# Kernel tuning notes

Measured on AMD Instinct MI355X. Metric: run time of the kernel, lower is better.

The kernel has to match this reference:

```python
import jax, jax.numpy as jnp
import numpy as np

N = 100000   # cells per k-dimension
C = 64       # input channels per dim
H = 128      # hidden dim
NNZ = 800000 # nonzeros per sparse matrix (avg degree 8)


def spmm(r, c, v, x):
    # y = A @ x for COO A with rows r, cols c, vals v; x: [N, H]
    return jax.ops.segment_sum(v[:, None] * x[c], r, num_segments=x.shape[0])


def spmm_t(r, c, v, y):
    # z = A.T @ y
    return jax.ops.segment_sum(v[:, None] * y[r], c, num_segments=y.shape[0])


def encoder(xs, params, adjs, B1, B2):
    # HierarchicalMessagePassing over k-dims 0..2; boundary_down[k]=B_k, boundary_up[k]=B_{k+1}
    bdown = (None, B1, B2)
    bup = (B1, B2, None)
    outs = []
    for d in range(3):
        W, b, a = params[d]
        xt = xs[d] @ W + b                                   # [N, H]
        ar, ac, av = adjs[d]
        comb = spmm(ar, ac, av, xt)                          # same-dim messages
        if bdown[d] is not None:
            r, c, v = bdown[d]
            comb = comb + 0.5 * spmm_t(r, c, v, spmm(r, c, v, xt))
        if bup[d] is not None:
            r, c, v = bup[d]
            comb = comb + 0.5 * spmm_t(r, c, v, spmm(r, c, v, xt))
        gate = jax.nn.sigmoid(comb @ a)                      # [N] sigmoid attention
        outs.append(gate[:, None] * comb)
    return jnp.mean(jnp.stack(outs, 0), 0)                   # mean over k-dims


def setup_inputs() -> dict:
    key = jax.random.key(0)
    ks = iter(jax.random.split(key, 64))
    d = {}
    for i in range(3):
        d[f"x{i}"] = jax.random.normal(next(ks), (N, C), jnp.float32)
    for nm in ("a0", "a1", "a2", "b1", "b2"):
        d[nm + "r"] = jax.random.randint(next(ks), (NNZ,), 0, N, jnp.int32)
        d[nm + "c"] = jax.random.randint(next(ks), (NNZ,), 0, N, jnp.int32)
        d[nm + "v"] = jax.random.uniform(next(ks), (NNZ,), jnp.float32)
    sw = 1.0 / np.sqrt(C)
    sh = 1.0 / np.sqrt(H)
    for tag in ("o", "t"):
        for i in range(3):
            d[f"W{tag}{i}"] = jax.random.normal(next(ks), (C, H), jnp.float32) * sw
            d[f"b{tag}{i}"] = jnp.zeros((H,), jnp.float32)
            d[f"a{tag}{i}"] = jax.random.normal(next(ks), (H,), jnp.float32) * 0.1
    d["pW1"] = jax.random.normal(next(ks), (H, H), jnp.float32) * sh
    d["pb1"] = jnp.zeros((H,), jnp.float32)
    d["alpha"] = jnp.full((1,), 0.25, jnp.float32)  # PReLU default
    d["pW2"] = jax.random.normal(next(ks), (H, H), jnp.float32) * sh
    d["pb2"] = jnp.zeros((H,), jnp.float32)
    return d


def reference(x0, x1, x2, a0r, a0c, a0v, a1r, a1c, a1v, a2r, a2c, a2v,
              b1r, b1c, b1v, b2r, b2c, b2v,
              Wo0, bo0, ao0, Wo1, bo1, ao1, Wo2, bo2, ao2,
              Wt0, bt0, at0, Wt1, bt1, at1, Wt2, bt2, at2,
              pW1, pb1, alpha, pW2, pb2):
    xs = (x0, x1, x2)
    adjs = ((a0r, a0c, a0v), (a1r, a1c, a1v), (a2r, a2c, a2v))
    B1 = (b1r, b1c, b1v)
    B2 = (b2r, b2c, b2v)
    h_online = encoder(xs, ((Wo0, bo0, ao0), (Wo1, bo1, ao1), (Wo2, bo2, ao2)), adjs, B1, B2)
    h1 = h_online @ pW1 + pb1
    h1 = jnp.where(h1 >= 0, h1, alpha * h1)  # PReLU
    h_pred = h1 @ pW2 + pb2
    h_target = jax.lax.stop_gradient(
        encoder(xs, ((Wt0, bt0, at0), (Wt1, bt1, at1), (Wt2, bt2, at2)), adjs, B1, B2))
    return h_online, h_pred, h_target
```

## Files before the change

kernel.cpp:

```cpp
#include <hip/hip_runtime.h>
#include <cstddef>

#define NCELL 100000
#define NNZE  800000
#define HID   128
#define CIN   64
#define T7    (7 * NCELL)
#define KPB   512
#define NBKT  196
#define TOTB  (7 * NBKT)

struct P7i { const int* p[7]; };
struct P7f { const float* p[7]; };

__device__ __forceinline__ unsigned short f2bf(float f) {
  unsigned u = __float_as_uint(f);
  return (unsigned short)((u + 0x7fffu + ((u >> 16) & 1u)) >> 16);
}
__device__ __forceinline__ float bflo(unsigned x) { return __uint_as_float(x << 16); }
__device__ __forceinline__ float bfhi(unsigned x) { return __uint_as_float(x & 0xffff0000u); }
__device__ __forceinline__ void fma4(float4& a, float s, const float4& w) {
  a.x += s * w.x; a.y += s * w.y; a.z += s * w.z; a.w += s * w.w;
}


__global__ __launch_bounds__(256) void bhist(P7i keys, int* __restrict__ bhcnt) {
  __shared__ int h[NBKT];
  int s = blockIdx.y;
  int t = threadIdx.x;
  if (t < NBKT) h[t] = 0;
  __syncthreads();
  const int* kp = keys.p[s];
  for (int j = 0; j < 64; ++j) {
    int i = blockIdx.x * 16384 + j * 256 + t;
    if (i < NNZE) atomicAdd(&h[kp[i] >> 9], 1);
  }
  __syncthreads();
  if (t < NBKT && h[t]) atomicAdd(&bhcnt[s * NBKT + t], h[t]);
}

__global__ __launch_bounds__(256) void bscan(const int* __restrict__ bh,
                                             int* __restrict__ boff,
                                             int* __restrict__ bcur,
                                             int* __restrict__ rowp) {
  __shared__ int ss[256];
  int t = threadIdx.x;
  int v[6];
  int s = 0;
  for (int j = 0; j < 6; ++j) {
    int idx = t * 6 + j;
    v[j] = s;
    s += (idx < TOTB) ? bh[idx] : 0;
  }
  ss[t] = s;
  __syncthreads();
  for (int off = 1; off < 256; off <<= 1) {
    int w = (t >= off) ? ss[t - off] : 0;
    __syncthreads();
    ss[t] += w;
    __syncthreads();
  }
  int excl = ss[t] - s;
  for (int j = 0; j < 6; ++j) {
    int idx = t * 6 + j;
    if (idx < TOTB) {
      int o = excl + v[j];
      boff[idx] = o;
      bcur[idx * 16] = o;
    }
  }
  if (t == 255) boff[TOTB] = ss[255];
  if (t == 0) rowp[T7] = 7 * NNZE;
}

__global__ __launch_bounds__(256) void sortA(P7i keys, P7i oth, P7f vs,
                                             int* __restrict__ bcur,
                                             uint2* __restrict__ tmp) {
  int s = blockIdx.y;
  int t = threadIdx.x;
  const int* kp = keys.p[s];
  const int* op = oth.p[s];
  const float* vp = vs.p[s];
  for (int j = 0; j < 64; ++j) {
    int i = blockIdx.x * 16384 + j * 256 + t;
    if (i < NNZE) {
      int k = kp[i];
      int b = k >> 9;
      int pos = atomicAdd(&bcur[(s * NBKT + b) * 16], 1);
      unsigned hi = (unsigned)op[i] | ((unsigned)(k & 511) << 17);
      tmp[pos] = make_uint2((unsigned)__float_as_int(vp[i]), hi);
    }
  }
}

__global__ __launch_bounds__(256) void sortB(const uint2* __restrict__ tmp,
                                             const int* __restrict__ boff,
                                             int* __restrict__ rowp,
                                             int2* __restrict__ cv) {
  __shared__ int hist[KPB];
  __shared__ int ss[256];
  int t = threadIdx.x;
  int b = blockIdx.x, s = blockIdx.y;
  int tb = s * NBKT + b;
  int base = boff[tb];
  int cnt = boff[tb + 1] - base;
  int key0 = b * KPB;
  int nk = NCELL - key0; if (nk > KPB) nk = KPB;
  hist[t] = 0;
  hist[t + 256] = 0;
  __syncthreads();
  for (int i = t; i < cnt; i += 256)
    atomicAdd(&hist[tmp[base + i].y >> 17], 1);
  __syncthreads();
  int a0 = hist[2 * t], a1 = hist[2 * t + 1];
  int sum = a0 + a1;
  ss[t] = sum;
  __syncthreads();
  for (int off = 1; off < 256; off <<= 1) {
    int w = (t >= off) ? ss[t - off] : 0;
    __syncthreads();
    ss[t] += w;
    __syncthreads();
  }
  int excl = ss[t] - sum;
  hist[2 * t] = excl;
  hist[2 * t + 1] = excl + a0;
  __syncthreads();
  for (int k = t; k < nk; k += 256)
    rowp[s * NCELL + key0 + k] = base + hist[k];
  __syncthreads();
  for (int i = t; i < cnt; i += 256) {
    uint2 u = tmp[base + i];
    int k = u.y >> 17;
    int pos = atomicAdd(&hist[k], 1);
    cv[base + pos] = make_int2((int)(u.y & 0x1FFFFu), (int)u.x);
  }
}

template <int MODE>
__global__ __launch_bounds__(256) void spmm256(const int* __restrict__ rowp,
                                               const int2* __restrict__ cv,
                                               const uint2* __restrict__ xb,
                                               uint2* __restrict__ outT,
                                               float4* __restrict__ c0,
                                               float4* __restrict__ c1,
                                               const float4* __restrict__ g0p,
                                               const float4* __restrict__ g1p,
                                               float4* __restrict__ hon,
                                               float4* __restrict__ htg,
                                               int first) {
  int wid = (blockIdx.x * 256 + threadIdx.x) >> 6;
  int lane = threadIdx.x & 63;
  int s = rowp[wid], e = rowp[wid + 1];
  float a0 = 0.f, a1 = 0.f, a2 = 0.f, a3 = 0.f;
  int i = s;
  for (; i + 4 <= e; i += 4) {
    int2 p0 = cv[i], p1 = cv[i + 1], p2 = cv[i + 2], p3 = cv[i + 3];
    float v0 = __int_as_float(p0.y), v1 = __int_as_float(p1.y);
    float v2 = __int_as_float(p2.y), v3 = __int_as_float(p3.y);
    uint2 g0 = xb[(size_t)p0.x * 64 + lane];
    uint2 g1 = xb[(size_t)p1.x * 64 + lane];
    uint2 g2 = xb[(size_t)p2.x * 64 + lane];
    uint2 g3 = xb[(size_t)p3.x * 64 + lane];
    a0 += v0 * bflo(g0.x); a1 += v0 * bfhi(g0.x); a2 += v0 * bflo(g0.y); a3 += v0 * bfhi(g0.y);
    a0 += v1 * bflo(g1.x); a1 += v1 * bfhi(g1.x); a2 += v1 * bflo(g1.y); a3 += v1 * bfhi(g1.y);
    a0 += v2 * bflo(g2.x); a1 += v2 * bfhi(g2.x); a2 += v2 * bflo(g2.y); a3 += v2 * bfhi(g2.y);
    a0 += v3 * bflo(g3.x); a1 += v3 * bfhi(g3.x); a2 += v3 * bflo(g3.y); a3 += v3 * bfhi(g3.y);
  }
  for (; i < e; ++i) {
    int2 p = cv[i];
    float v = __int_as_float(p.y);
    uint2 g = xb[(size_t)p.x * 64 + lane];
    a0 += v * bflo(g.x); a1 += v * bfhi(g.x); a2 += v * bflo(g.y); a3 += v * bfhi(g.y);
  }
  if (MODE == 0) {
    uint2 pk;
    pk.x = (unsigned)f2bf(a0) | ((unsigned)f2bf(a1) << 16);
    pk.y = (unsigned)f2bf(a2) | ((unsigned)f2bf(a3) << 16);
    outT[(size_t)wid * 64 + lane] = pk;
  } else if (MODE == 1 || MODE == 2) {
    float4 v = make_float4(a0, a1, a2, a3);
    float4* dst = (lane < 32) ? (c0 + (size_t)wid * 32 + lane)
                              : (c1 + (size_t)wid * 32 + (lane - 32));
    if (MODE == 1) {
      *dst = v;
    } else {
      float4 cur = *dst;
      cur.x += 0.5f * v.x; cur.y += 0.5f * v.y;
      cur.z += 0.5f * v.z; cur.w += 0.5f * v.w;
      *dst = cur;
    }
  } else {
    bool e1 = lane >= 32;
    int l = lane & 31;
    const float4* cb = e1 ? c1 : c0;
    float4 cur = cb[(size_t)wid * 32 + l];
    cur.x += 0.5f * a0; cur.y += 0.5f * a1;
    cur.z += 0.5f * a2; cur.w += 0.5f * a3;
    float4 avv = (e1 ? g1p : g0p)[l];
    float d = cur.x * avv.x + cur.y * avv.y + cur.z * avv.z + cur.w * avv.w;
    d += __shfl_xor(d, 16);
    d += __shfl_xor(d, 8);
    d += __shfl_xor(d, 4);
    d += __shfl_xor(d, 2);
    d += __shfl_xor(d, 1);
    float g = (1.f / (1.f + __expf(-d))) * (1.f / 3.f);
    float4* hb = e1 ? htg : hon;
    size_t oi = (size_t)wid * 32 + l;
    float4 v = make_float4(g * cur.x, g * cur.y, g * cur.z, g * cur.w);
    if (first) {
      hb[oi] = v;
    } else {
      float4 c = hb[oi];
      c.x += v.x; c.y += v.y; c.z += v.z; c.w += v.w;
      hb[oi] = c;
    }
  }
}

__global__ __launch_bounds__(256) void gemm_nc2(const float* __restrict__ x,
                                                const float* __restrict__ W0,
                                                const float* __restrict__ b0,
                                                const float* __restrict__ W1,
                                                const float* __restrict__ b1,
                                                uint2* __restrict__ out) {
  __shared__ float xs[16][64];
  int t = threadIdx.x;
  int row0 = blockIdx.x * 16;
  ((float4*)xs)[t] = ((const float4*)x)[(size_t)row0 * 16 + t];
  __syncthreads();
  int tx = t & 31, ty = t >> 5;
  const float4* W0_4 = (const float4*)W0;
  const float4* W1_4 = (const float4*)W1;
  float4 a00 = {0, 0, 0, 0}, a01 = {0, 0, 0, 0}, a10 = {0, 0, 0, 0}, a11 = {0, 0, 0, 0};
#pragma unroll 8
  for (int k = 0; k < 64; ++k) {
    float xv0 = xs[ty][k];
    float xv1 = xs[ty + 8][k];
    float4 w0 = W0_4[k * 32 + tx];
    float4 w1 = W1_4[k * 32 + tx];
    fma4(a00, xv0, w0); fma4(a01, xv1, w0);
    fma4(a10, xv0, w1); fma4(a11, xv1, w1);
  }
  float4 bb0 = ((const float4*)b0)[tx];
  float4 bb1 = ((const float4*)b1)[tx];
  fma4(a00, 1.f, bb0); fma4(a01, 1.f, bb0);
  fma4(a10, 1.f, bb1); fma4(a11, 1.f, bb1);
  auto pack = [](const float4& v) {
    uint2 p;
    p.x = (unsigned)f2bf(v.x) | ((unsigned)f2bf(v.y) << 16);
    p.y = (unsigned)f2bf(v.z) | ((unsigned)f2bf(v.w) << 16);
    return p;
  };
  size_t r0 = (size_t)(row0 + ty) * 64;
  size_t r1 = (size_t)(row0 + ty + 8) * 64;
  out[r0 + tx] = pack(a00);
  out[r0 + 32 + tx] = pack(a10);
  out[r1 + tx] = pack(a01);
  out[r1 + 32 + tx] = pack(a11);
}

template <bool PRELU>
__global__ __launch_bounds__(256) void gemm_hh2(const float* __restrict__ x,
                                                const float* __restrict__ W,
                                                const float* __restrict__ b,
                                                const float* __restrict__ alpha,
                                                float* __restrict__ out) {
  __shared__ float As[32 * 36];
  __shared__ float Ws[32 * 128];
  int t = threadIdx.x;
  int tx = t & 31, ty = t >> 5;
  int row0 = blockIdx.x * 32;
  float4 acc[4] = {{0, 0, 0, 0}, {0, 0, 0, 0}, {0, 0, 0, 0}, {0, 0, 0, 0}};
  const float4* Wg4 = (const float4*)W;
  for (int kt = 0; kt < 4; ++kt) {
    __syncthreads();
    {
      int r = t >> 3;
      int c4 = t & 7;
      float4 av = ((const float4*)(x + (size_t)(row0 + r) * 128 + kt * 32))[c4];
      As[(c4 * 4 + 0) * 36 + r] = av.x;
      As[(c4 * 4 + 1) * 36 + r] = av.y;
      As[(c4 * 4 + 2) * 36 + r] = av.z;
      As[(c4 * 4 + 3) * 36 + r] = av.w;
    }
    {
#pragma unroll
      for (int j = 0; j < 4; ++j) {
        int idx = j * 256 + t;
        ((float4*)Ws)[idx] = Wg4[kt * 1024 + idx];
      }
    }
    __syncthreads();
#pragma unroll
    for (int k = 0; k < 32; ++k) {
      float4 am = *(const float4*)&As[k * 36 + ty * 4];
      float4 w4 = ((const float4*)Ws)[k * 32 + tx];
      fma4(acc[0], am.x, w4);
      fma4(acc[1], am.y, w4);
      fma4(acc[2], am.z, w4);
      fma4(acc[3], am.w, w4);
    }
  }
  float4 bb = ((const float4*)b)[tx];
  float al = PRELU ? alpha[0] : 0.f;
#pragma unroll
  for (int r = 0; r < 4; ++r) {
    float4 v = acc[r];
    v.x += bb.x; v.y += bb.y; v.z += bb.z; v.w += bb.w;
    if (PRELU) {
      v.x = v.x >= 0.f ? v.x : al * v.x;
      v.y = v.y >= 0.f ? v.y : al * v.y;
      v.z = v.z >= 0.f ? v.z : al * v.z;
      v.w = v.w >= 0.f ? v.w : al * v.w;
    }
    ((float4*)out)[(size_t)(row0 + ty * 4 + r) * 32 + tx] = v;
  }
}

extern "C" void kernel_launch(void* const* d_in, const int* in_sizes, int n_in,
                              void* d_out, int out_size, void* d_ws, size_t ws_size,
                              hipStream_t stream) {
  const float* x[3] = {(const float*)d_in[0], (const float*)d_in[1], (const float*)d_in[2]};
  const int* kr[5]; const int* kc[5]; const float* kv[5];
  for (int m = 0; m < 5; ++m) {
    kr[m] = (const int*)d_in[3 + 3 * m];
    kc[m] = (const int*)d_in[4 + 3 * m];
    kv[m] = (const float*)d_in[5 + 3 * m];
  }
  const float *W[2][3], *bv[2][3], *av[2][3];
  int idx = 18;
  for (int e = 0; e < 2; ++e)
    for (int d = 0; d < 3; ++d) {
      W[e][d] = (const float*)d_in[idx++];
      bv[e][d] = (const float*)d_in[idx++];
      av[e][d] = (const float*)d_in[idx++];
    }
  const float* pW1 = (const float*)d_in[36];
  const float* pb1 = (const float*)d_in[37];
  const float* alpha = (const float*)d_in[38];
  const float* pW2 = (const float*)d_in[39];
  const float* pb2 = (const float*)d_in[40];

  float* out = (float*)d_out;
  const size_t NH = (size_t)NCELL * HID;
  float* h_online = out;
  float* h_pred = out + NH;
  float* h_target = out + 2 * NH;

  char* w = (char*)d_ws;
  auto carve = [&](size_t bytes) -> void* {
    void* p = (void*)w;
    w += (bytes + 255) & ~(size_t)255;
    return p;
  };
  int* rowp_g = (int*)carve((size_t)(T7 + 1) * 4);
  int2* cv_g = (int2*)carve((size_t)7 * NNZE * 8);
  int* bhcnt = (int*)carve((size_t)TOTB * 4);
  int* boff = (int*)carve((size_t)(TOTB + 1) * 4);
  int* bcur = (int*)carve((size_t)TOTB * 16 * 4);
  uint2* xt2 = (uint2*)carve((size_t)NCELL * 256 * 2);
  uint2* t2 = (uint2*)carve((size_t)NCELL * 256 * 2);
  float* comb1 = (float*)carve(NH * 4);
  float* comb0 = h_pred;
  uint2* tmp = t2;

  P7i skey = {{kr[0], kr[1], kr[2], kr[3], kc[3], kr[4], kc[4]}};
  P7i soth = {{kc[0], kc[1], kc[2], kc[3], kr[3], kc[4], kr[4]}};
  P7f sval = {{kv[0], kv[1], kv[2], kv[3], kv[3], kv[4], kv[4]}};

  hipMemsetAsync(bhcnt, 0, (size_t)TOTB * 4, stream);
  bhist<<<dim3(49, 7), 256, 0, stream>>>(skey, bhcnt);
  bscan<<<1, 256, 0, stream>>>(bhcnt, boff, bcur, rowp_g);
  sortA<<<dim3(49, 7), 256, 0, stream>>>(skey, soth, sval, bcur, tmp);
  sortB<<<dim3(NBKT, 7), 256, 0, stream>>>(tmp, boff, rowp_g, cv_g);

  static const int nB[3] = {1, 2, 1};
  static const int BS[3][2] = {{3, -1}, {3, 5}, {5, -1}};
  for (int d = 0; d < 3; ++d) {
    gemm_nc2<<<6250, 256, 0, stream>>>(x[d], W[0][d], bv[0][d], W[1][d], bv[1][d], xt2);
    spmm256<1><<<25000, 256, 0, stream>>>(rowp_g + d * NCELL, cv_g, xt2,
                                          nullptr, (float4*)comb0, (float4*)comb1,
                                          nullptr, nullptr, nullptr, nullptr, 0);
    for (int bi = 0; bi < nB[d]; ++bi) {
      int sR = BS[d][bi];
      spmm256<0><<<25000, 256, 0, stream>>>(rowp_g + sR * NCELL, cv_g, xt2,
                                            t2, nullptr, nullptr,
                                            nullptr, nullptr, nullptr, nullptr, 0);
      if (bi == nB[d] - 1) {
        spmm256<3><<<25000, 256, 0, stream>>>(rowp_g + (sR + 1) * NCELL, cv_g, t2,
                                              nullptr, (float4*)comb0, (float4*)comb1,
                                              (const float4*)av[0][d], (const float4*)av[1][d],
                                              (float4*)h_online, (float4*)h_target,
                                              d == 0 ? 1 : 0);
      } else {
        spmm256<2><<<25000, 256, 0, stream>>>(rowp_g + (sR + 1) * NCELL, cv_g, t2,
                                              nullptr, (float4*)comb0, (float4*)comb1,
                                              nullptr, nullptr, nullptr, nullptr, 0);
      }
    }
  }

  float* tmpf = (float*)t2;
  gemm_hh2<true><<<3125, 256, 0, stream>>>(h_online, pW1, pb1, alpha, tmpf);
  gemm_hh2<false><<<3125, 256, 0, stream>>>(tmpf, pW2, pb2, alpha, h_pred);
}
```

Baseline: 1.923 ms.

## Fuse same-dim and boundary SpMM chains into one gating kernel; per-block sort offsets

The same-dimension SpMM and the transpose-side boundary SpMMs are merged into a single kernel that accumulates everything in registers before applying the sigmoid gate. This removes the fp32 comb intermediate buffers and their read-modify-write traffic, and it cuts the number of kernel launches. Dim 1 now needs a second bf16 temporary buffer. The bucket sort also switches from global atomics on bucket cursors to per-block histograms with a single-block prefix scan. That adds a serial scan over about 67k entries in exchange.

```diff
diff --git a/kernel.cpp b/kernel.cpp
--- a/kernel.cpp
+++ b/kernel.cpp
@@ -9,6 +9,7 @@
 #define KPB   512
 #define NBKT  196
 #define TOTB  (7 * NBKT)
+#define NBLK  49
 
 struct P7i { const int* p[7]; };
 struct P7f { const float* p[7]; };
@@ -24,33 +25,30 @@
 }
 
 
-__global__ __launch_bounds__(256) void bhist(P7i keys, int* __restrict__ bhcnt) {
+__global__ __launch_bounds__(256) void phist(P7i keys, int* __restrict__ bh) {
   __shared__ int h[NBKT];
-  int s = blockIdx.y;
-  int t = threadIdx.x;
+  int s = blockIdx.y, blk = blockIdx.x, t = threadIdx.x;
   if (t < NBKT) h[t] = 0;
   __syncthreads();
   const int* kp = keys.p[s];
   for (int j = 0; j < 64; ++j) {
-    int i = blockIdx.x * 16384 + j * 256 + t;
+    int i = blk * 16384 + j * 256 + t;
     if (i < NNZE) atomicAdd(&h[kp[i] >> 9], 1);
   }
   __syncthreads();
-  if (t < NBKT && h[t]) atomicAdd(&bhcnt[s * NBKT + t], h[t]);
-}
-
-__global__ __launch_bounds__(256) void bscan(const int* __restrict__ bh,
-                                             int* __restrict__ boff,
-                                             int* __restrict__ bcur,
-                                             int* __restrict__ rowp) {
+  if (t < NBKT) bh[(s * NBKT + t) * NBLK + blk] = h[t];
+}
+
+__global__ __launch_bounds__(256) void pscan(int* __restrict__ bh) {
   __shared__ int ss[256];
+  const int n = TOTB * NBLK;
+  const int CH = 263;
   int t = threadIdx.x;
-  int v[6];
+  int base = t * CH;
   int s = 0;
-  for (int j = 0; j < 6; ++j) {
-    int idx = t * 6 + j;
-    v[j] = s;
-    s += (idx < TOTB) ? bh[idx] : 0;
+  for (int j = 0; j < CH; ++j) {
+    int idx = base + j;
+    if (idx < n) s += bh[idx];
   }
   ss[t] = s;
   __syncthreads();
@@ -60,35 +58,45 @@
     ss[t] += w;
     __syncthreads();
   }
-  int excl = ss[t] - s;
-  for (int j = 0; j < 6; ++j) {
-    int idx = t * 6 + j;
-    if (idx < TOTB) {
-      int o = excl + v[j];
-      boff[idx] = o;
-      bcur[idx * 16] = o;
-    }
-  }
-  if (t == 255) boff[TOTB] = ss[255];
-  if (t == 0) rowp[T7] = 7 * NNZE;
-}
-
-__global__ __launch_bounds__(256) void sortA(P7i keys, P7i oth, P7f vs,
-                                             int* __restrict__ bcur,
-                                             uint2* __restrict__ tmp) {
-  int s = blockIdx.y;
-  int t = threadIdx.x;
+  int run = ss[t] - s;
+  for (int j = 0; j < CH; ++j) {
+    int idx = base + j;
+    if (idx < n) {
+      int v = bh[idx];
+      bh[idx] = run;
+      run += v;
+    }
+  }
+}
+
+__global__ __launch_bounds__(256) void pboff(const int* __restrict__ bofs,
+                                             int* __restrict__ boff,
+                                             int* __restrict__ rowp) {
+  int i = blockIdx.x * 256 + threadIdx.x;
+  if (i < TOTB) boff[i] = bofs[i * NBLK];
+  if (i == 0) {
+    boff[TOTB] = 7 * NNZE;
+    rowp[T7] = 7 * NNZE;
+  }
+}
+
+__global__ __launch_bounds__(256) void pscatter(P7i keys, P7i oth, P7f vs,
+                                                const int* __restrict__ bofs,
+                                                uint2* __restrict__ tmp) {
+  __shared__ int cur[NBKT];
+  int s = blockIdx.y, blk = blockIdx.x, t = threadIdx.x;
+  if (t < NBKT) cur[t] = bofs[(s * NBKT + t) * NBLK + blk];
+  __syncthreads();
   const int* kp = keys.p[s];
   const int* op = oth.p[s];
   const float* vp = vs.p[s];
   for (int j = 0; j < 64; ++j) {
-    int i = blockIdx.x * 16384 + j * 256 + t;
+    int i = blk * 16384 + j * 256 + t;
     if (i < NNZE) {
       int k = kp[i];
-      int b = k >> 9;
-      int pos = atomicAdd(&bcur[(s * NBKT + b) * 16], 1);
-      unsigned hi = (unsigned)op[i] | ((unsigned)(k & 511) << 17);
-      tmp[pos] = make_uint2((unsigned)__float_as_int(vp[i]), hi);
+      int pos = atomicAdd(&cur[k >> 9], 1);
+      tmp[pos] = make_uint2((unsigned)__float_as_int(vp[i]),
+                            (unsigned)op[i] | ((unsigned)(k & 511) << 17));
     }
   }
 }
@@ -137,27 +145,16 @@
   }
 }
 
-template <int MODE>
-__global__ __launch_bounds__(256) void spmm256(const int* __restrict__ rowp,
-                                               const int2* __restrict__ cv,
-                                               const uint2* __restrict__ xb,
-                                               uint2* __restrict__ outT,
-                                               float4* __restrict__ c0,
-                                               float4* __restrict__ c1,
-                                               const float4* __restrict__ g0p,
-                                               const float4* __restrict__ g1p,
-                                               float4* __restrict__ hon,
-                                               float4* __restrict__ htg,
-                                               int first) {
-  int wid = (blockIdx.x * 256 + threadIdx.x) >> 6;
-  int lane = threadIdx.x & 63;
+__device__ __forceinline__ void gather4(const int* __restrict__ rowp, int wid, int lane,
+                                        const int2* __restrict__ cv,
+                                        const uint2* __restrict__ xb, float wgt,
+                                        float& a0, float& a1, float& a2, float& a3) {
   int s = rowp[wid], e = rowp[wid + 1];
-  float a0 = 0.f, a1 = 0.f, a2 = 0.f, a3 = 0.f;
   int i = s;
   for (; i + 4 <= e; i += 4) {
     int2 p0 = cv[i], p1 = cv[i + 1], p2 = cv[i + 2], p3 = cv[i + 3];
-    float v0 = __int_as_float(p0.y), v1 = __int_as_float(p1.y);
-    float v2 = __int_as_float(p2.y), v3 = __int_as_float(p3.y);
+    float v0 = wgt * __int_as_float(p0.y), v1 = wgt * __int_as_float(p1.y);
+    float v2 = wgt * __int_as_float(p2.y), v3 = wgt * __int_as_float(p3.y);
     uint2 g0 = xb[(size_t)p0.x * 64 + lane];
     uint2 g1 = xb[(size_t)p1.x * 64 + lane];
     uint2 g2 = xb[(size_t)p2.x * 64 + lane];
@@ -169,52 +166,65 @@
   }
   for (; i < e; ++i) {
     int2 p = cv[i];
-    float v = __int_as_float(p.y);
+    float v = wgt * __int_as_float(p.y);
     uint2 g = xb[(size_t)p.x * 64 + lane];
     a0 += v * bflo(g.x); a1 += v * bfhi(g.x); a2 += v * bflo(g.y); a3 += v * bfhi(g.y);
   }
-  if (MODE == 0) {
-    uint2 pk;
-    pk.x = (unsigned)f2bf(a0) | ((unsigned)f2bf(a1) << 16);
-    pk.y = (unsigned)f2bf(a2) | ((unsigned)f2bf(a3) << 16);
-    outT[(size_t)wid * 64 + lane] = pk;
-  } else if (MODE == 1 || MODE == 2) {
-    float4 v = make_float4(a0, a1, a2, a3);
-    float4* dst = (lane < 32) ? (c0 + (size_t)wid * 32 + lane)
-                              : (c1 + (size_t)wid * 32 + (lane - 32));
-    if (MODE == 1) {
-      *dst = v;
-    } else {
-      float4 cur = *dst;
-      cur.x += 0.5f * v.x; cur.y += 0.5f * v.y;
-      cur.z += 0.5f * v.z; cur.w += 0.5f * v.w;
-      *dst = cur;
-    }
+}
+
+__global__ __launch_bounds__(256) void spmm_b(const int* __restrict__ rowp,
+                                              const int2* __restrict__ cv,
+                                              const uint2* __restrict__ xb,
+                                              uint2* __restrict__ outT) {
+  int wid = (blockIdx.x * 256 + threadIdx.x) >> 6;
+  int lane = threadIdx.x & 63;
+  float a0 = 0.f, a1 = 0.f, a2 = 0.f, a3 = 0.f;
+  gather4(rowp, wid, lane, cv, xb, 1.f, a0, a1, a2, a3);
+  uint2 pk;
+  pk.x = (unsigned)f2bf(a0) | ((unsigned)f2bf(a1) << 16);
+  pk.y = (unsigned)f2bf(a2) | ((unsigned)f2bf(a3) << 16);
+  outT[(size_t)wid * 64 + lane] = pk;
+}
+
+template <int NCHAIN>
+__global__ __launch_bounds__(256) void spmm_mega(const int* __restrict__ rowpA,
+                                                 const int* __restrict__ rowpT0,
+                                                 const int* __restrict__ rowpT1,
+                                                 const int2* __restrict__ cv,
+                                                 const uint2* __restrict__ xb,
+                                                 const uint2* __restrict__ t0,
+                                                 const uint2* __restrict__ t1,
+                                                 const float4* __restrict__ g0p,
+                                                 const float4* __restrict__ g1p,
+                                                 float4* __restrict__ hon,
+                                                 float4* __restrict__ htg,
+                                                 int first) {
+  int wid = (blockIdx.x * 256 + threadIdx.x) >> 6;
+  int lane = threadIdx.x & 63;
+  float a0 = 0.f, a1 = 0.f, a2 = 0.f, a3 = 0.f;
+  gather4(rowpA, wid, lane, cv, xb, 1.f, a0, a1, a2, a3);
+  gather4(rowpT0, wid, lane, cv, t0, 0.5f, a0, a1, a2, a3);
+  if (NCHAIN == 2) gather4(rowpT1, wid, lane, cv, t1, 0.5f, a0, a1, a2, a3);
+
+  bool e1 = lane >= 32;
+  int l = lane & 31;
+  float4 avv = (e1 ? g1p : g0p)[l];
+  float d = a0 * avv.x + a1 * avv.y + a2 * avv.z + a3 * avv.w;
+  d += __shfl_xor(d, 16);
+  d += __shfl_xor(d, 8);
+  d += __shfl_xor(d, 4);
+  d += __shfl_xor(d, 2);
+  d += __shfl_xor(d, 1);
+  float g = (1.f / (1.f + __expf(-d))) * (1.f / 3.f);
+  float4* hb = e1 ? htg : hon;
+  size_t oi = (size_t)wid * 32 + l;
+  float4 v = make_float4(g * a0, g * a1, g * a2, g * a3);
+  if (first) {
+    hb[oi] = v;
   } else {
-    bool e1 = lane >= 32;
-    int l = lane & 31;
-    const float4* cb = e1 ? c1 : c0;
-    float4 cur = cb[(size_t)wid * 32 + l];
-    cur.x += 0.5f * a0; cur.y += 0.5f * a1;
-    cur.z += 0.5f * a2; cur.w += 0.5f * a3;
-    float4 avv = (e1 ? g1p : g0p)[l];
-    float d = cur.x * avv.x + cur.y * avv.y + cur.z * avv.z + cur.w * avv.w;
-    d += __shfl_xor(d, 16);
-    d += __shfl_xor(d, 8);
-    d += __shfl_xor(d, 4);
-    d += __shfl_xor(d, 2);
-    d += __shfl_xor(d, 1);
-    float g = (1.f / (1.f + __expf(-d))) * (1.f / 3.f);
-    float4* hb = e1 ? htg : hon;
-    size_t oi = (size_t)wid * 32 + l;
-    float4 v = make_float4(g * cur.x, g * cur.y, g * cur.z, g * cur.w);
-    if (first) {
-      hb[oi] = v;
-    } else {
-      float4 c = hb[oi];
-      c.x += v.x; c.y += v.y; c.z += v.z; c.w += v.w;
-      hb[oi] = c;
-    }
+    float4 c = hb[oi];
+    c.x += v.x; c.y += v.y; c.z += v.z; c.w += v.w;
+    hb[oi] = c;
   }
 }
 
@@ -356,52 +366,46 @@
   };
   int* rowp_g = (int*)carve((size_t)(T7 + 1) * 4);
   int2* cv_g = (int2*)carve((size_t)7 * NNZE * 8);
-  int* bhcnt = (int*)carve((size_t)TOTB * 4);
+  int* bh = (int*)carve((size_t)TOTB * NBLK * 4);
   int* boff = (int*)carve((size_t)(TOTB + 1) * 4);
-  int* bcur = (int*)carve((size_t)TOTB * 16 * 4);
   uint2* xt2 = (uint2*)carve((size_t)NCELL * 256 * 2);
-  uint2* t2 = (uint2*)carve((size_t)NCELL * 256 * 2);
-  float* comb1 = (float*)carve(NH * 4);
-  float* comb0 = h_pred;
-  uint2* tmp = t2;
+  uint2* t2a = (uint2*)carve((size_t)NCELL * 256 * 2);
+  uint2* t2b = (uint2*)carve((size_t)NCELL * 256 * 2);
+  uint2* tmp = t2a;
 
   P7i skey = {{kr[0], kr[1], kr[2], kr[3], kc[3], kr[4], kc[4]}};
   P7i soth = {{kc[0], kc[1], kc[2], kc[3], kr[3], kc[4], kr[4]}};
   P7f sval = {{kv[0], kv[1], kv[2], kv[3], kv[3], kv[4], kv[4]}};
 
-  hipMemsetAsync(bhcnt, 0, (size_t)TOTB * 4, stream);
-  bhist<<<dim3(49, 7), 256, 0, stream>>>(skey, bhcnt);
-  bscan<<<1, 256, 0, stream>>>(bhcnt, boff, bcur, rowp_g);
-  sortA<<<dim3(49, 7), 256, 0, stream>>>(skey, soth, sval, bcur, tmp);
+  phist<<<dim3(NBLK, 7), 256, 0, stream>>>(skey, bh);
+  pscan<<<1, 256, 0, stream>>>(bh);
+  pboff<<<6, 256, 0, stream>>>(bh, boff, rowp_g);
+  pscatter<<<dim3(NBLK, 7), 256, 0, stream>>>(skey, soth, sval, bh, tmp);
   sortB<<<dim3(NBKT, 7), 256, 0, stream>>>(tmp, boff, rowp_g, cv_g);
 
-  static const int nB[3] = {1, 2, 1};
-  static const int BS[3][2] = {{3, -1}, {3, 5}, {5, -1}};
-  for (int d = 0; d < 3; ++d) {
-    gemm_nc2<<<6250, 256, 0, stream>>>(x[d], W[0][d], bv[0][d], W[1][d], bv[1][d], xt2);
-    spmm256<1><<<25000, 256, 0, stream>>>(rowp_g + d * NCELL, cv_g, xt2,
-                                          nullptr, (float4*)comb0, (float4*)comb1,
-                                          nullptr, nullptr, nullptr, nullptr, 0);
-    for (int bi = 0; bi < nB[d]; ++bi) {
-      int sR = BS[d][bi];
-      spmm256<0><<<25000, 256, 0, stream>>>(rowp_g + sR * NCELL, cv_g, xt2,
-                                            t2, nullptr, nullptr,
-                                            nullptr, nullptr, nullptr, nullptr, 0);
-      if (bi == nB[d] - 1) {
-        spmm256<3><<<25000, 256, 0, stream>>>(rowp_g + (sR + 1) * NCELL, cv_g, t2,
-                                              nullptr, (float4*)comb0, (float4*)comb1,
-                                              (const float4*)av[0][d], (const float4*)av[1][d],
-                                              (float4*)h_online, (float4*)h_target,
-                                              d == 0 ? 1 : 0);
-      } else {
-        spmm256<2><<<25000, 256, 0, stream>>>(rowp_g + (sR + 1) * NCELL, cv_g, t2,
-                                              nullptr, (float4*)comb0, (float4*)comb1,
-                                              nullptr, nullptr, nullptr, nullptr, 0);
-      }
-    }
-  }
-
-  float* tmpf = (float*)t2;
+  gemm_nc2<<<6250, 256, 0, stream>>>(x[0], W[0][0], bv[0][0], W[1][0], bv[1][0], xt2);
+  spmm_b<<<25000, 256, 0, stream>>>(rowp_g + 3 * NCELL, cv_g, xt2, t2a);
+  spmm_mega<1><<<25000, 256, 0, stream>>>(rowp_g + 0 * NCELL, rowp_g + 4 * NCELL, nullptr,
+                                          cv_g, xt2, t2a, nullptr,
+                                          (const float4*)av[0][0], (const float4*)av[1][0],
+                                          (float4*)h_online, (float4*)h_target, 1);
+
+  gemm_nc2<<<6250, 256, 0, stream>>>(x[1], W[0][1], bv[0][1], W[1][1], bv[1][1], xt2);
+  spmm_b<<<25000, 256, 0, stream>>>(rowp_g + 3 * NCELL, cv_g, xt2, t2a);
+  spmm_b<<<25000, 256, 0, stream>>>(rowp_g + 5 * NCELL, cv_g, xt2, t2b);
+  spmm_mega<2><<<25000, 256, 0, stream>>>(rowp_g + 1 * NCELL, rowp_g + 4 * NCELL,
+                                          rowp_g + 6 * NCELL, cv_g, xt2, t2a, t2b,
+                                          (const float4*)av[0][1], (const float4*)av[1][1],
+                                          (float4*)h_online, (float4*)h_target, 0);
+
+  gemm_nc2<<<6250, 256, 0, stream>>>(x[2], W[0][2], bv[0][2], W[1][2], bv[1][2], xt2);
+  spmm_b<<<25000, 256, 0, stream>>>(rowp_g + 5 * NCELL, cv_g, xt2, t2a);
+  spmm_mega<1><<<25000, 256, 0, stream>>>(rowp_g + 2 * NCELL, rowp_g + 6 * NCELL, nullptr,
+                                          cv_g, xt2, t2a, nullptr,
+                                          (const float4*)av[0][2], (const float4*)av[1][2],
+                                          (float4*)h_online, (float4*)h_target, 0);
+
+  float* tmpf = (float*)t2a;
   gemm_hh2<true><<<3125, 256, 0, stream>>>(h_online, pW1, pb1, alpha, tmpf);
   gemm_hh2<false><<<3125, 256, 0, stream>>>(tmpf, pW2, pb2, alpha, h_pred);
 }
```

Measured after the change: 1.721 ms. 1.12x faster.
